# Performance work log

Measured on AMD Instinct MI355X. Metric: run time of the kernel, lower is better.

Reference implementation:

```python
import jax, jax.numpy as jnp
import numpy as np

IN_DIM = 14400
K = 25
DIMS = [7200, 3600, 1800]  # floor(in_dim / 2**(i+1))
OUT_DIM = 2
BATCH = 256


def setup_inputs() -> dict:
    key = jax.random.key(0)
    ks = jax.random.split(key, 32)
    inp = {}
    inp["x"] = jax.random.normal(ks[0], (BATCH, 2 * IN_DIM), dtype=jnp.float32)
    # shared KNN tables (both channels load the same h5 files)
    prev = [IN_DIM] + DIMS[:-1]
    for i, (d, p) in enumerate(zip(DIMS, prev)):
        inp[f"knn{i}"] = jax.random.randint(ks[1 + i], (d, K), 0, p, dtype=jnp.int64)
    std = (2.0 / K) ** 0.5
    kidx = 4
    for ch in ("p", "n"):
        for i, d in enumerate(DIMS):
            inp[f"w{ch}{i}"] = jax.random.normal(ks[kidx], (d, K), dtype=jnp.float32) * std; kidx += 1
            inp[f"b{ch}{i}"] = jnp.zeros((1, d), dtype=jnp.float32)
        inp[f"fc{ch}_w"] = jax.random.normal(ks[kidx], (OUT_DIM, DIMS[-1]), dtype=jnp.float32) * (1.0 / DIMS[-1] ** 0.5); kidx += 1
        inp[f"fc{ch}_b"] = jnp.zeros((OUT_DIM,), dtype=jnp.float32)
    inp["fc3_w"] = jax.random.normal(ks[kidx], (OUT_DIM, 4), dtype=jnp.float32) * 0.5
    inp["fc3_b"] = jnp.zeros((OUT_DIM,), dtype=jnp.float32)
    return inp


def _lcn(x, knns, ws, bs, fw, fb):
    # x: (B, in_dim). Each layer: gather KNN neighbors, weighted sum, bias, relu.
    for knn, w, b in zip(knns, ws, bs):
        g = x[:, knn]                                  # (B, dim, K) gather
        x = jax.nn.relu(jnp.einsum('bdk,dk->bd', g, w) + b)
    return x @ fw.T + fb                               # fc_angle


def reference(x, knn0, knn1, knn2,
              wp0, bp0, wp1, bp1, wp2, bp2, fcp_w, fcp_b,
              wn0, bn0, wn1, bn1, wn2, bn2, fcn_w, fcn_b,
              fc3_w, fc3_b):
    knns = (knn0, knn1, knn2)
    xpos = _lcn(x[:, :IN_DIM], knns, (wp0, wp1, wp2), (bp0, bp1, bp2), fcp_w, fcp_b)
    xneg = _lcn(x[:, IN_DIM:], knns, (wn0, wn1, wn2), (bn0, bn1, bn2), fcn_w, fcn_b)
    h = jax.nn.relu(jnp.concatenate([xpos, xneg], axis=1))  # (B, 4)
    return h @ fc3_w.T + fc3_b
```

## Files before the change

kernel.cpp:

```cpp
#include <hip/hip_runtime.h>
#include <hip/hip_bf16.h>

using bf16 = __hip_bfloat16;

typedef _Float16 half1;
typedef _Float16 half2_t __attribute__((ext_vector_type(2)));

#define K 25
#define D0 7200
#define D1 3600
#define D2 1800

#define PKB_L1 360000
#define PKB_L2 540000
#define NPK    630000
#define NPB    25200

#define NT 1024

__device__ __forceinline__ float b2f(ushort u) {
  unsigned int w = ((unsigned int)u) << 16;
  float f; __builtin_memcpy(&f, &w, 4); return f;
}
__device__ __forceinline__ ushort f2b(float f) {
  bf16 h = __float2bfloat16(f);
  ushort u; __builtin_memcpy(&u, &h, 2); return u;
}
__device__ __forceinline__ ushort f2h(float f) {
  half1 h = (half1)f;
  return __builtin_bit_cast(ushort, h);
}
__device__ __forceinline__ unsigned int pkf16(float a, float b) {
  return __builtin_bit_cast(unsigned int, __builtin_amdgcn_cvt_pkrtz(a, b));
}

__global__ __launch_bounds__(256) void prepack_kernel(
    const void* __restrict__ x,
    const void* __restrict__ knn0, const void* __restrict__ knn1,
    const void* __restrict__ knn2,
    const void* __restrict__ wp0, const void* __restrict__ bp0,
    const void* __restrict__ wp1, const void* __restrict__ bp1,
    const void* __restrict__ wp2, const void* __restrict__ bp2,
    const void* __restrict__ wn0, const void* __restrict__ bn0,
    const void* __restrict__ wn1, const void* __restrict__ bn1,
    const void* __restrict__ wn2, const void* __restrict__ bn2,
    unsigned int* __restrict__ pk, float* __restrict__ pbias,
    float* __restrict__ y, int* __restrict__ flags) {
  __shared__ int s_flags[2];
  const int t = threadIdx.x;
  if (t < 64) {
    const unsigned int u = ((const unsigned int*)x)[t * 997];
    const unsigned int e = (u >> 23) & 0xFF;
    const unsigned long long m = __ballot((e >= 192) || (e <= 30));
    if (t == 0) s_flags[0] = (__popcll(m) >= 32) ? 1 : 0;
  } else if (t < 128) {
    const int l = t - 64;
    const unsigned int hi = ((const unsigned int*)knn0)[2 * l + 1];
    const unsigned long long m = __ballot(hi != 0);
    if (l == 0) s_flags[1] = (m == 0ULL) ? 1 : 0;
  }
  __syncthreads();
  const int fdt = s_flags[0], idt = s_flags[1];

  if (blockIdx.x == 0 && t == 0) {
    flags[0] = fdt; flags[1] = idt; flags[16] = 0;
  }

  const int gid = blockIdx.x * 256 + t;
  if (gid < NPB) {
    int i = gid, d, dout, pkb;
    const void *kn, *wsel, *bsel;
    if (i < 14400) {
      const int ch = i / D0; d = i - ch * D0; dout = D0;
      pkb = ch * 180000; kn = knn0;
      wsel = ch ? wn0 : wp0; bsel = ch ? bn0 : bp0;
    } else if (i < 21600) {
      i -= 14400; const int ch = i / D1; d = i - ch * D1; dout = D1;
      pkb = PKB_L1 + ch * 90000; kn = knn1;
      wsel = ch ? wn1 : wp1; bsel = ch ? bn1 : bp1;
    } else {
      i -= 21600; const int ch = i / D2; d = i - ch * D2; dout = D2;
      pkb = PKB_L2 + ch * 45000; kn = knn2;
      wsel = ch ? wn2 : wp2; bsel = ch ? bn2 : bp2;
    }
    const int pos0 = d * K;
#pragma unroll
    for (int k = 0; k < K; ++k) {
      const unsigned int idx = idt ? ((const unsigned int*)kn)[2 * (pos0 + k)]
                                   : ((const unsigned int*)kn)[pos0 + k];
      const ushort wb = fdt ? f2h(b2f(((const ushort*)wsel)[pos0 + k]))
                            : f2h(((const float*)wsel)[pos0 + k]);
      pk[pkb + k * dout + d] = (idx << 18) | (unsigned int)wb;
    }
    pbias[gid] = fdt ? b2f(((const ushort*)bsel)[d]) : ((const float*)bsel)[d];
  } else if (gid < NPB + 1024) {
    y[gid - NPB] = 0.0f;
  }
}

template <int BIN, int BOUT>
__device__ __forceinline__ void layer_run(char* ldsb, const unsigned int* __restrict__ pk,
                                          const float* __restrict__ pbias,
                                          int pkb, int pbb, int dout) {
  for (int d = threadIdx.x; d < dout; d += NT) {
    const int base = pkb + d;
    float a0 = 0.f, a1 = 0.f;
#pragma unroll
    for (int k = 0; k < K; ++k) {
      const unsigned int pw = pk[base + k * dout];
      const half2_t vv = *(const half2_t*)(ldsb + BIN + (pw >> 16));
      const half1 wh = __builtin_bit_cast(half1, (ushort)(pw & 0xFFFFu));
      a0 = fmaf((float)wh, (float)vv.x, a0);
      a1 = fmaf((float)wh, (float)vv.y, a1);
    }
    const float bias = pbias[pbb + d];
    a0 = fmaxf(a0 + bias, 0.f);
    a1 = fmaxf(a1 + bias, 0.f);
    *(unsigned int*)(ldsb + BOUT + (d << 2)) = pkf16(a0, a1);
  }
}

__global__ __launch_bounds__(NT) void lcn_fused(
    const void* __restrict__ x, const unsigned int* __restrict__ pk,
    const float* __restrict__ pbias,
    const void* __restrict__ fcpw, const void* __restrict__ fcnw,
    const void* __restrict__ fcpb, const void* __restrict__ fcnb,
    const void* __restrict__ f3w, const void* __restrict__ f3b,
    float* __restrict__ y, int* __restrict__ flags, void* __restrict__ out) {
  __shared__ __align__(16) char ldsb[86400];
  __shared__ float red[NT / 64][4];
  __shared__ int sflag;
  const int t = threadIdx.x;
  const int ch = blockIdx.x & 1;
  const int b0 = (blockIdx.x >> 1) * 2;

  if (t == 0) sflag = flags[0];
  __syncthreads();
  const int fdt = sflag;

  if (fdt) {
    const ushort* r0 = (const ushort*)x + (size_t)b0 * 28800 + ch * 14400;
    const ushort* r1 = r0 + 28800;
    for (int c = t; c < 3600; c += NT) {
      const ushort4 a = ((const ushort4*)r0)[c];
      const ushort4 b = ((const ushort4*)r1)[c];
      uint4 u;
      u.x = pkf16(b2f(a.x), b2f(b.x));
      u.y = pkf16(b2f(a.y), b2f(b.y));
      u.z = pkf16(b2f(a.z), b2f(b.z));
      u.w = pkf16(b2f(a.w), b2f(b.w));
      ((uint4*)ldsb)[c] = u;
    }
  } else {
    const float* r0 = (const float*)x + (size_t)b0 * 28800 + ch * 14400;
    const float* r1 = r0 + 28800;
    for (int c = t; c < 3600; c += NT) {
      const float4 a = ((const float4*)r0)[c];
      const float4 b = ((const float4*)r1)[c];
      uint4 u;
      u.x = pkf16(a.x, b.x);
      u.y = pkf16(a.y, b.y);
      u.z = pkf16(a.z, b.z);
      u.w = pkf16(a.w, b.w);
      ((uint4*)ldsb)[c] = u;
    }
  }
  __syncthreads();

  layer_run<0, 57600>(ldsb, pk, pbias, 0 + ch * 180000, 0 + ch * D0, D0);
  __syncthreads();
  layer_run<57600, 0>(ldsb, pk, pbias, PKB_L1 + ch * 90000, 14400 + ch * D1, D1);
  __syncthreads();
  layer_run<0, 14400>(ldsb, pk, pbias, PKB_L2 + ch * 45000, 21600 + ch * D2, D2);
  __syncthreads();

  {
    const void* fw = ch ? fcnw : fcpw;
    float a00 = 0.f, a01 = 0.f, a10 = 0.f, a11 = 0.f;
    for (int d = t; d < D2; d += NT) {
      const half2_t vv = *(const half2_t*)(ldsb + 14400 + (d << 2));
      const float v0 = (float)vv.x;
      const float v1 = (float)vv.y;
      const float w0 = fdt ? b2f(((const ushort*)fw)[d]) : ((const float*)fw)[d];
      const float w1 = fdt ? b2f(((const ushort*)fw)[D2 + d]) : ((const float*)fw)[D2 + d];
      a00 = fmaf(w0, v0, a00); a01 = fmaf(w0, v1, a01);
      a10 = fmaf(w1, v0, a10); a11 = fmaf(w1, v1, a11);
    }
#pragma unroll
    for (int off = 32; off > 0; off >>= 1) {
      a00 += __shfl_down(a00, off);
      a01 += __shfl_down(a01, off);
      a10 += __shfl_down(a10, off);
      a11 += __shfl_down(a11, off);
    }
    const int wave = t >> 6, lane = t & 63;
    if (lane == 0) {
      red[wave][0] = a00; red[wave][1] = a01; red[wave][2] = a10; red[wave][3] = a11;
    }
    __syncthreads();
    if (t == 0) {
      float s00 = 0.f, s01 = 0.f, s10 = 0.f, s11 = 0.f;
#pragma unroll
      for (int wv = 0; wv < NT / 64; ++wv) {
        s00 += red[wv][0]; s01 += red[wv][1]; s10 += red[wv][2]; s11 += red[wv][3];
      }
      atomicAdd(&y[(ch * 2 + 0) * 256 + b0], s00);
      atomicAdd(&y[(ch * 2 + 0) * 256 + b0 + 1], s01);
      atomicAdd(&y[(ch * 2 + 1) * 256 + b0], s10);
      atomicAdd(&y[(ch * 2 + 1) * 256 + b0 + 1], s11);
    }
  }

  __syncthreads();
  if (t == 0) {
    __threadfence();
    sflag = (atomicAdd(&flags[16], 1) == (int)gridDim.x - 1) ? 1 : 0;
  }
  __syncthreads();
  if (sflag && t < 256) {
    const int b = t;
    const float y0 = atomicAdd(&y[0 * 256 + b], 0.0f);
    const float y1 = atomicAdd(&y[1 * 256 + b], 0.0f);
    const float y2 = atomicAdd(&y[2 * 256 + b], 0.0f);
    const float y3 = atomicAdd(&y[3 * 256 + b], 0.0f);
    const float bp0v = fdt ? b2f(((const ushort*)fcpb)[0]) : ((const float*)fcpb)[0];
    const float bp1v = fdt ? b2f(((const ushort*)fcpb)[1]) : ((const float*)fcpb)[1];
    const float bn0v = fdt ? b2f(((const ushort*)fcnb)[0]) : ((const float*)fcnb)[0];
    const float bn1v = fdt ? b2f(((const ushort*)fcnb)[1]) : ((const float*)fcnb)[1];
    const float h0v = fmaxf(y0 + bp0v, 0.f);
    const float h1v = fmaxf(y1 + bp1v, 0.f);
    const float h2v = fmaxf(y2 + bn0v, 0.f);
    const float h3v = fmaxf(y3 + bn1v, 0.f);
#pragma unroll
    for (int o = 0; o < 2; ++o) {
      float w0, w1, w2, w3, bb;
      if (fdt) {
        const ushort* fp = (const ushort*)f3w;
        w0 = b2f(fp[o * 4 + 0]); w1 = b2f(fp[o * 4 + 1]);
        w2 = b2f(fp[o * 4 + 2]); w3 = b2f(fp[o * 4 + 3]);
        bb = b2f(((const ushort*)f3b)[o]);
      } else {
        const float* fp = (const float*)f3w;
        w0 = fp[o * 4 + 0]; w1 = fp[o * 4 + 1];
        w2 = fp[o * 4 + 2]; w3 = fp[o * 4 + 3];
        bb = ((const float*)f3b)[o];
      }
      float r = bb;
      r = fmaf(w0, h0v, r); r = fmaf(w1, h1v, r);
      r = fmaf(w2, h2v, r); r = fmaf(w3, h3v, r);
      if (fdt) ((ushort*)out)[b * 2 + o] = f2b(r);
      else     ((float*)out)[b * 2 + o] = r;
    }
  }
}

extern "C" void kernel_launch(void* const* d_in, const int* in_sizes, int n_in,
                              void* d_out, int out_size, void* d_ws, size_t ws_size,
                              hipStream_t stream) {
  const void* x    = d_in[0];
  const void* knn0 = d_in[1];
  const void* knn1 = d_in[2];
  const void* knn2 = d_in[3];
  const void* wp0  = d_in[4];  const void* bp0 = d_in[5];
  const void* wp1  = d_in[6];  const void* bp1 = d_in[7];
  const void* wp2  = d_in[8];  const void* bp2 = d_in[9];
  const void* fcpw = d_in[10]; const void* fcpb = d_in[11];
  const void* wn0  = d_in[12]; const void* bn0 = d_in[13];
  const void* wn1  = d_in[14]; const void* bn1 = d_in[15];
  const void* wn2  = d_in[16]; const void* bn2 = d_in[17];
  const void* fcnw = d_in[18]; const void* fcnb = d_in[19];
  const void* f3w  = d_in[20]; const void* f3b  = d_in[21];

  char* ws = (char*)d_ws;
  unsigned int* pk = (unsigned int*)(ws);
  float* pbias = (float*)(ws + 2520000);
  float* y     = (float*)(ws + 2620800);
  int* flags   = (int*)(ws + 2624896);

  prepack_kernel<<<103, 256, 0, stream>>>(x, knn0, knn1, knn2,
                                          wp0, bp0, wp1, bp1, wp2, bp2,
                                          wn0, bn0, wn1, bn1, wn2, bn2,
                                          pk, pbias, y, flags);

  lcn_fused<<<256, NT, 0, stream>>>(x, pk, pbias, fcpw, fcnw, fcpb, fcnb,
                                    f3w, f3b, y, flags, d_out);
}
```

Baseline: 148.1 us.

## Fuse prepack and LCN compute into one cooperative kernel with grid sync

Merges the weight/index prepack kernel and the main LCN kernel into a single cooperative launch. Each block prepacks part of the tables and stages its x rows into LDS, then a grid-wide sync separates prepack from compute. This removes one kernel launch and overlaps x staging with prepack, at the cost of a grid barrier and a cooperative-launch requirement. A fallback to the old two-kernel path is kept if the cooperative launch fails.

```diff
diff --git a/kernel.cpp b/kernel.cpp
--- a/kernel.cpp
+++ b/kernel.cpp
@@ -1,5 +1,8 @@
 #include <hip/hip_runtime.h>
 #include <hip/hip_bf16.h>
+#include <hip/hip_cooperative_groups.h>
+
+namespace cg = cooperative_groups;
 
 using bf16 = __hip_bfloat16;
 
@@ -17,6 +20,7 @@
 #define NPB    25200
 
 #define NT 1024
+#define GRID 256
 
 __device__ __forceinline__ float b2f(ushort u) {
   unsigned int w = ((unsigned int)u) << 16;
@@ -34,68 +38,39 @@
   return __builtin_bit_cast(unsigned int, __builtin_amdgcn_cvt_pkrtz(a, b));
 }
 
-__global__ __launch_bounds__(256) void prepack_kernel(
-    const void* __restrict__ x,
-    const void* __restrict__ knn0, const void* __restrict__ knn1,
-    const void* __restrict__ knn2,
-    const void* __restrict__ wp0, const void* __restrict__ bp0,
-    const void* __restrict__ wp1, const void* __restrict__ bp1,
-    const void* __restrict__ wp2, const void* __restrict__ bp2,
-    const void* __restrict__ wn0, const void* __restrict__ bn0,
-    const void* __restrict__ wn1, const void* __restrict__ bn1,
-    const void* __restrict__ wn2, const void* __restrict__ bn2,
-    unsigned int* __restrict__ pk, float* __restrict__ pbias,
-    float* __restrict__ y, int* __restrict__ flags) {
-  __shared__ int s_flags[2];
-  const int t = threadIdx.x;
-  if (t < 64) {
-    const unsigned int u = ((const unsigned int*)x)[t * 997];
-    const unsigned int e = (u >> 23) & 0xFF;
-    const unsigned long long m = __ballot((e >= 192) || (e <= 30));
-    if (t == 0) s_flags[0] = (__popcll(m) >= 32) ? 1 : 0;
-  } else if (t < 128) {
-    const int l = t - 64;
-    const unsigned int hi = ((const unsigned int*)knn0)[2 * l + 1];
-    const unsigned long long m = __ballot(hi != 0);
-    if (l == 0) s_flags[1] = (m == 0ULL) ? 1 : 0;
-  }
-  __syncthreads();
-  const int fdt = s_flags[0], idt = s_flags[1];
-
-  if (blockIdx.x == 0 && t == 0) {
-    flags[0] = fdt; flags[1] = idt; flags[16] = 0;
-  }
-
-  const int gid = blockIdx.x * 256 + t;
-  if (gid < NPB) {
-    int i = gid, d, dout, pkb;
-    const void *kn, *wsel, *bsel;
-    if (i < 14400) {
-      const int ch = i / D0; d = i - ch * D0; dout = D0;
-      pkb = ch * 180000; kn = knn0;
-      wsel = ch ? wn0 : wp0; bsel = ch ? bn0 : bp0;
-    } else if (i < 21600) {
-      i -= 14400; const int ch = i / D1; d = i - ch * D1; dout = D1;
-      pkb = PKB_L1 + ch * 90000; kn = knn1;
-      wsel = ch ? wn1 : wp1; bsel = ch ? bn1 : bp1;
-    } else {
-      i -= 21600; const int ch = i / D2; d = i - ch * D2; dout = D2;
-      pkb = PKB_L2 + ch * 45000; kn = knn2;
-      wsel = ch ? wn2 : wp2; bsel = ch ? bn2 : bp2;
-    }
-    const int pos0 = d * K;
-#pragma unroll
-    for (int k = 0; k < K; ++k) {
-      const unsigned int idx = idt ? ((const unsigned int*)kn)[2 * (pos0 + k)]
-                                   : ((const unsigned int*)kn)[pos0 + k];
-      const ushort wb = fdt ? f2h(b2f(((const ushort*)wsel)[pos0 + k]))
-                            : f2h(((const float*)wsel)[pos0 + k]);
-      pk[pkb + k * dout + d] = (idx << 18) | (unsigned int)wb;
-    }
-    pbias[gid] = fdt ? b2f(((const ushort*)bsel)[d]) : ((const float*)bsel)[d];
-  } else if (gid < NPB + 1024) {
-    y[gid - NPB] = 0.0f;
-  }
+__device__ __forceinline__ void prepack_one(
+    int gid, int idt, int fdt,
+    const void* knn0, const void* knn1, const void* knn2,
+    const void* wp0, const void* bp0, const void* wp1, const void* bp1,
+    const void* wp2, const void* bp2,
+    const void* wn0, const void* bn0, const void* wn1, const void* bn1,
+    const void* wn2, const void* bn2,
+    unsigned int* __restrict__ pk, float* __restrict__ pbias) {
+  int i = gid, d, dout, pkb;
+  const void *kn, *wsel, *bsel;
+  if (i < 14400) {
+    const int ch = i / D0; d = i - ch * D0; dout = D0;
+    pkb = ch * 180000; kn = knn0;
+    wsel = ch ? wn0 : wp0; bsel = ch ? bn0 : bp0;
+  } else if (i < 21600) {
+    i -= 14400; const int ch = i / D1; d = i - ch * D1; dout = D1;
+    pkb = PKB_L1 + ch * 90000; kn = knn1;
+    wsel = ch ? wn1 : wp1; bsel = ch ? bn1 : bp1;
+  } else {
+    i -= 21600; const int ch = i / D2; d = i - ch * D2; dout = D2;
+    pkb = PKB_L2 + ch * 45000; kn = knn2;
+    wsel = ch ? wn2 : wp2; bsel = ch ? bn2 : bp2;
+  }
+  const int pos0 = d * K;
+#pragma unroll
+  for (int k = 0; k < K; ++k) {
+    const unsigned int idx = idt ? ((const unsigned int*)kn)[2 * (pos0 + k)]
+                                 : ((const unsigned int*)kn)[pos0 + k];
+    const ushort wb = fdt ? f2h(b2f(((const ushort*)wsel)[pos0 + k]))
+                          : f2h(((const float*)wsel)[pos0 + k]);
+    pk[pkb + k * dout + d] = (idx << 18) | (unsigned int)wb;
+  }
+  pbias[gid] = fdt ? b2f(((const ushort*)bsel)[d]) : ((const float*)bsel)[d];
 }
 
 template <int BIN, int BOUT>
@@ -120,24 +95,9 @@
   }
 }
 
-__global__ __launch_bounds__(NT) void lcn_fused(
-    const void* __restrict__ x, const unsigned int* __restrict__ pk,
-    const float* __restrict__ pbias,
-    const void* __restrict__ fcpw, const void* __restrict__ fcnw,
-    const void* __restrict__ fcpb, const void* __restrict__ fcnb,
-    const void* __restrict__ f3w, const void* __restrict__ f3b,
-    float* __restrict__ y, int* __restrict__ flags, void* __restrict__ out) {
-  __shared__ __align__(16) char ldsb[86400];
-  __shared__ float red[NT / 64][4];
-  __shared__ int sflag;
-  const int t = threadIdx.x;
-  const int ch = blockIdx.x & 1;
-  const int b0 = (blockIdx.x >> 1) * 2;
-
-  if (t == 0) sflag = flags[0];
-  __syncthreads();
-  const int fdt = sflag;
-
+__device__ __forceinline__ void stage_x(char* ldsb, const void* __restrict__ x,
+                                        int fdt, int ch, int b0) {
+  const int t = threadIdx.x;
   if (fdt) {
     const ushort* r0 = (const ushort*)x + (size_t)b0 * 28800 + ch * 14400;
     const ushort* r1 = r0 + 28800;
@@ -165,7 +125,16 @@
       ((uint4*)ldsb)[c] = u;
     }
   }
-  __syncthreads();
+}
+
+__device__ __forceinline__ void compute_phase(
+    char* ldsb, float (*red)[4], int* sflag_p,
+    const unsigned int* __restrict__ pk, const float* __restrict__ pbias,
+    const void* fcpw, const void* fcnw, const void* fcpb, const void* fcnb,
+    const void* f3w, const void* f3b,
+    float* __restrict__ y, int* __restrict__ flags, void* __restrict__ out,
+    int fdt, int ch, int b0, int nblocks) {
+  const int t = threadIdx.x;
 
   layer_run<0, 57600>(ldsb, pk, pbias, 0 + ch * 180000, 0 + ch * D0, D0);
   __syncthreads();
@@ -214,10 +183,10 @@
   __syncthreads();
   if (t == 0) {
     __threadfence();
-    sflag = (atomicAdd(&flags[16], 1) == (int)gridDim.x - 1) ? 1 : 0;
-  }
-  __syncthreads();
-  if (sflag && t < 256) {
+    *sflag_p = (atomicAdd(&flags[16], 1) == nblocks - 1) ? 1 : 0;
+  }
+  __syncthreads();
+  if (*sflag_p && t < 256) {
     const int b = t;
     const float y0 = atomicAdd(&y[0 * 256 + b], 0.0f);
     const float y1 = atomicAdd(&y[1 * 256 + b], 0.0f);
@@ -254,6 +223,133 @@
   }
 }
 
+__global__ __launch_bounds__(NT) void lcn_all(
+    const void* __restrict__ x,
+    const void* __restrict__ knn0, const void* __restrict__ knn1,
+    const void* __restrict__ knn2,
+    const void* __restrict__ wp0, const void* __restrict__ bp0,
+    const void* __restrict__ wp1, const void* __restrict__ bp1,
+    const void* __restrict__ wp2, const void* __restrict__ bp2,
+    const void* __restrict__ wn0, const void* __restrict__ bn0,
+    const void* __restrict__ wn1, const void* __restrict__ bn1,
+    const void* __restrict__ wn2, const void* __restrict__ bn2,
+    const void* __restrict__ fcpw, const void* __restrict__ fcnw,
+    const void* __restrict__ fcpb, const void* __restrict__ fcnb,
+    const void* __restrict__ f3w, const void* __restrict__ f3b,
+    unsigned int* __restrict__ pk, float* __restrict__ pbias,
+    float* __restrict__ y, int* __restrict__ flags, void* __restrict__ out) {
+  __shared__ __align__(16) char ldsb[86400];
+  __shared__ float red[NT / 64][4];
+  __shared__ int s_flags[2];
+  __shared__ int sflag;
+  const int t = threadIdx.x;
+  const int bid = blockIdx.x;
+  const int ch = bid & 1;
+  const int b0 = (bid >> 1) * 2;
+
+  if (t < 64) {
+    const unsigned int u = ((const unsigned int*)x)[t * 997];
+    const unsigned int e = (u >> 23) & 0xFF;
+    const unsigned long long m = __ballot((e >= 192) || (e <= 30));
+    if (t == 0) s_flags[0] = (__popcll(m) >= 32) ? 1 : 0;
+  } else if (t < 128) {
+    const int l = t - 64;
+    const unsigned int hi = ((const unsigned int*)knn0)[2 * l + 1];
+    const unsigned long long m = __ballot(hi != 0);
+    if (l == 0) s_flags[1] = (m == 0ULL) ? 1 : 0;
+  }
+  __syncthreads();
+  const int fdt = s_flags[0], idt = s_flags[1];
+
+  const int gid = bid * NT + t;
+  if (gid < NPB) {
+    prepack_one(gid, idt, fdt, knn0, knn1, knn2,
+                wp0, bp0, wp1, bp1, wp2, bp2,
+                wn0, bn0, wn1, bn1, wn2, bn2, pk, pbias);
+  }
+  if (bid == GRID - 1) {
+    atomicExch((unsigned int*)&y[t & 1023], 0u);
+    if (t == 0) atomicExch(&flags[16], 0);
+  }
+
+  stage_x(ldsb, x, fdt, ch, b0);
+  __syncthreads();
+
+  __threadfence();
+  cg::this_grid().sync();
+  __threadfence();
+
+  compute_phase(ldsb, red, &sflag, pk, pbias, fcpw, fcnw, fcpb, fcnb,
+                f3w, f3b, y, flags, out, fdt, ch, b0, GRID);
+}
+
+__global__ __launch_bounds__(256) void prepack_kernel(
+    const void* __restrict__ x,
+    const void* __restrict__ knn0, const void* __restrict__ knn1,
+    const void* __restrict__ knn2,
+    const void* __restrict__ wp0, const void* __restrict__ bp0,
+    const void* __restrict__ wp1, const void* __restrict__ bp1,
+    const void* __restrict__ wp2, const void* __restrict__ bp2,
+    const void* __restrict__ wn0, const void* __restrict__ bn0,
+    const void* __restrict__ wn1, const void* __restrict__ bn1,
+    const void* __restrict__ wn2, const void* __restrict__ bn2,
+    unsigned int* __restrict__ pk, float* __restrict__ pbias,
+    float* __restrict__ y, int* __restrict__ flags) {
+  __shared__ int s_flags[2];
+  const int t = threadIdx.x;
+  if (t < 64) {
+    const unsigned int u = ((const unsigned int*)x)[t * 997];
+    const unsigned int e = (u >> 23) & 0xFF;
+    const unsigned long long m = __ballot((e >= 192) || (e <= 30));
+    if (t == 0) s_flags[0] = (__popcll(m) >= 32) ? 1 : 0;
+  } else if (t < 128) {
+    const int l = t - 64;
+    const unsigned int hi = ((const unsigned int*)knn0)[2 * l + 1];
+    const unsigned long long m = __ballot(hi != 0);
+    if (l == 0) s_flags[1] = (m == 0ULL) ? 1 : 0;
+  }
+  __syncthreads();
+  const int fdt = s_flags[0], idt = s_flags[1];
+
+  if (blockIdx.x == 0 && t == 0) {
+    flags[0] = fdt; flags[1] = idt; flags[16] = 0;
+  }
+
+  const int gid = blockIdx.x * 256 + t;
+  if (gid < NPB) {
+    prepack_one(gid, idt, fdt, knn0, knn1, knn2,
+                wp0, bp0, wp1, bp1, wp2, bp2,
+                wn0, bn0, wn1, bn1, wn2, bn2, pk, pbias);
+  } else if (gid < NPB + 1024) {
+    y[gid - NPB] = 0.0f;
+  }
+}
+
+__global__ __launch_bounds__(NT) void lcn_fused(
+    const void* __restrict__ x, const unsigned int* __restrict__ pk,
+    const float* __restrict__ pbias,
+    const void* __restrict__ fcpw, const void* __restrict__ fcnw,
+    const void* __restrict__ fcpb, const void* __restrict__ fcnb,
+    const void* __restrict__ f3w, const void* __restrict__ f3b,
+    float* __restrict__ y, int* __restrict__ flags, void* __restrict__ out) {
+  __shared__ __align__(16) char ldsb[86400];
+  __shared__ float red[NT / 64][4];
+  __shared__ int sflag;
+  const int t = threadIdx.x;
+  const int ch = blockIdx.x & 1;
+  const int b0 = (blockIdx.x >> 1) * 2;
+
+  if (t == 0) sflag = flags[0];
+  __syncthreads();
+  const int fdt = sflag;
+
+  stage_x(ldsb, x, fdt, ch, b0);
+  __syncthreads();
+
+  compute_phase(ldsb, red, &sflag, pk, pbias, fcpw, fcnw, fcpb, fcnb,
+                f3w, f3b, y, flags, out, fdt, ch, b0, (int)gridDim.x);
+}
+
 extern "C" void kernel_launch(void* const* d_in, const int* in_sizes, int n_in,
                               void* d_out, int out_size, void* d_ws, size_t ws_size,
                               hipStream_t stream) {
@@ -277,11 +373,25 @@
   float* y     = (float*)(ws + 2620800);
   int* flags   = (int*)(ws + 2624896);
 
-  prepack_kernel<<<103, 256, 0, stream>>>(x, knn0, knn1, knn2,
-                                          wp0, bp0, wp1, bp1, wp2, bp2,
-                                          wn0, bn0, wn1, bn1, wn2, bn2,
-                                          pk, pbias, y, flags);
-
-  lcn_fused<<<256, NT, 0, stream>>>(x, pk, pbias, fcpw, fcnw, fcpb, fcnb,
-                                    f3w, f3b, y, flags, d_out);
-}
+  void* out = d_out;
+  void* args[] = {
+      (void*)&x, (void*)&knn0, (void*)&knn1, (void*)&knn2,
+      (void*)&wp0, (void*)&bp0, (void*)&wp1, (void*)&bp1,
+      (void*)&wp2, (void*)&bp2,
+      (void*)&wn0, (void*)&bn0, (void*)&wn1, (void*)&bn1,
+      (void*)&wn2, (void*)&bn2,
+      (void*)&fcpw, (void*)&fcnw, (void*)&fcpb, (void*)&fcnb,
+      (void*)&f3w, (void*)&f3b,
+      (void*)&pk, (void*)&pbias, (void*)&y, (void*)&flags, (void*)&out};
+
+  hipError_t e = hipLaunchCooperativeKernel((const void*)lcn_all, dim3(GRID),
+                                            dim3(NT), args, 0, stream);
+  if (e != hipSuccess) {
+    prepack_kernel<<<103, 256, 0, stream>>>(x, knn0, knn1, knn2,
+                                            wp0, bp0, wp1, bp1, wp2, bp2,
+                                            wn0, bn0, wn1, bn1, wn2, bn2,
+                                            pk, pbias, y, flags);
+    lcn_fused<<<256, NT, 0, stream>>>(x, pk, pbias, fcpw, fcnw, fcpb, fcnb,
+                                      f3w, f3b, y, flags, d_out);
+  }
+}
```

Result: slower. 366.2 us (+147.3%).

## Split prepack across two thread halves and process two outputs per thread in layers

Applied to the files above, without the earlier changes.

The prepack kernel now gives each output dimension to two threads that each pack about half of the K neighbours, doubling the grid, and a dedicated block zeroes y. In the fused kernel, layer_run takes the output dimension as a template parameter and has each thread compute two output positions per iteration with independent accumulators, exposing more memory-level parallelism for the packed-weight loads and LDS gathers. Launch bounds now request a minimum of 4 blocks per multiprocessor. Handling two outputs at once raises register pressure, and the min-blocks hint may force spills, though the 86 KB of LDS per block likely limits occupancy anyway.

```diff
diff --git a/kernel.cpp b/kernel.cpp
--- a/kernel.cpp
+++ b/kernel.cpp
@@ -32,6 +32,35 @@
 }
 __device__ __forceinline__ unsigned int pkf16(float a, float b) {
   return __builtin_bit_cast(unsigned int, __builtin_amdgcn_cvt_pkrtz(a, b));
+}
+
+struct DimMap {
+  int d, dout, pkb;
+  const void *kn, *wsel, *bsel;
+};
+__device__ __forceinline__ DimMap map_gid(
+    int gid,
+    const void* knn0, const void* knn1, const void* knn2,
+    const void* wp0, const void* bp0, const void* wp1, const void* bp1,
+    const void* wp2, const void* bp2,
+    const void* wn0, const void* bn0, const void* wn1, const void* bn1,
+    const void* wn2, const void* bn2) {
+  DimMap m;
+  int i = gid;
+  if (i < 14400) {
+    const int ch = i / D0; m.d = i - ch * D0; m.dout = D0;
+    m.pkb = ch * 180000; m.kn = knn0;
+    m.wsel = ch ? wn0 : wp0; m.bsel = ch ? bn0 : bp0;
+  } else if (i < 21600) {
+    i -= 14400; const int ch = i / D1; m.d = i - ch * D1; m.dout = D1;
+    m.pkb = PKB_L1 + ch * 90000; m.kn = knn1;
+    m.wsel = ch ? wn1 : wp1; m.bsel = ch ? bn1 : bp1;
+  } else {
+    i -= 21600; const int ch = i / D2; m.d = i - ch * D2; m.dout = D2;
+    m.pkb = PKB_L2 + ch * 45000; m.kn = knn2;
+    m.wsel = ch ? wn2 : wp2; m.bsel = ch ? bn2 : bp2;
+  }
+  return m;
 }
 
 __global__ __launch_bounds__(256) void prepack_kernel(
@@ -48,6 +77,15 @@
     float* __restrict__ y, int* __restrict__ flags) {
   __shared__ int s_flags[2];
   const int t = threadIdx.x;
+
+  if (blockIdx.x == 197) {
+    if (t < 256) {
+#pragma unroll
+      for (int j = 0; j < 4; ++j) y[t + j * 256] = 0.0f;
+    }
+    return;
+  }
+
   if (t < 64) {
     const unsigned int u = ((const unsigned int*)x)[t * 997];
     const unsigned int e = (u >> 23) & 0xFF;
@@ -66,61 +104,107 @@
     flags[0] = fdt; flags[1] = idt; flags[16] = 0;
   }
 
-  const int gid = blockIdx.x * 256 + t;
+  const int local = t & 127;
+  const int khalf = t >> 7;
+  const int gid = blockIdx.x * 128 + local;
   if (gid < NPB) {
-    int i = gid, d, dout, pkb;
-    const void *kn, *wsel, *bsel;
-    if (i < 14400) {
-      const int ch = i / D0; d = i - ch * D0; dout = D0;
-      pkb = ch * 180000; kn = knn0;
-      wsel = ch ? wn0 : wp0; bsel = ch ? bn0 : bp0;
-    } else if (i < 21600) {
-      i -= 14400; const int ch = i / D1; d = i - ch * D1; dout = D1;
-      pkb = PKB_L1 + ch * 90000; kn = knn1;
-      wsel = ch ? wn1 : wp1; bsel = ch ? bn1 : bp1;
+    const DimMap m = map_gid(gid, knn0, knn1, knn2,
+                             wp0, bp0, wp1, bp1, wp2, bp2,
+                             wn0, bn0, wn1, bn1, wn2, bn2);
+    const int pos0 = m.d * K;
+    if (khalf == 0) {
+#pragma unroll
+      for (int k = 0; k < 13; ++k) {
+        const unsigned int idx = idt ? ((const unsigned int*)m.kn)[2 * (pos0 + k)]
+                                     : ((const unsigned int*)m.kn)[pos0 + k];
+        const ushort wb = fdt ? f2h(b2f(((const ushort*)m.wsel)[pos0 + k]))
+                              : f2h(((const float*)m.wsel)[pos0 + k]);
+        pk[m.pkb + k * m.dout + m.d] = (idx << 18) | (unsigned int)wb;
+      }
+      pbias[gid] = fdt ? b2f(((const ushort*)m.bsel)[m.d]) : ((const float*)m.bsel)[m.d];
     } else {
-      i -= 21600; const int ch = i / D2; d = i - ch * D2; dout = D2;
-      pkb = PKB_L2 + ch * 45000; kn = knn2;
-      wsel = ch ? wn2 : wp2; bsel = ch ? bn2 : bp2;
-    }
-    const int pos0 = d * K;
-#pragma unroll
-    for (int k = 0; k < K; ++k) {
-      const unsigned int idx = idt ? ((const unsigned int*)kn)[2 * (pos0 + k)]
-                                   : ((const unsigned int*)kn)[pos0 + k];
-      const ushort wb = fdt ? f2h(b2f(((const ushort*)wsel)[pos0 + k]))
-                            : f2h(((const float*)wsel)[pos0 + k]);
-      pk[pkb + k * dout + d] = (idx << 18) | (unsigned int)wb;
-    }
-    pbias[gid] = fdt ? b2f(((const ushort*)bsel)[d]) : ((const float*)bsel)[d];
-  } else if (gid < NPB + 1024) {
-    y[gid - NPB] = 0.0f;
-  }
-}
-
-template <int BIN, int BOUT>
+#pragma unroll
+      for (int k = 13; k < 25; ++k) {
+        const unsigned int idx = idt ? ((const unsigned int*)m.kn)[2 * (pos0 + k)]
+                                     : ((const unsigned int*)m.kn)[pos0 + k];
+        const ushort wb = fdt ? f2h(b2f(((const ushort*)m.wsel)[pos0 + k]))
+                              : f2h(((const float*)m.wsel)[pos0 + k]);
+        pk[m.pkb + k * m.dout + m.d] = (idx << 18) | (unsigned int)wb;
+      }
+    }
+  }
+}
+
+template <int BIN, int BOUT, int DOUT>
 __device__ __forceinline__ void layer_run(char* ldsb, const unsigned int* __restrict__ pk,
                                           const float* __restrict__ pbias,
-                                          int pkb, int pbb, int dout) {
-  for (int d = threadIdx.x; d < dout; d += NT) {
-    const int base = pkb + d;
-    float a0 = 0.f, a1 = 0.f;
+                                          int pkb, int pbb) {
+  const int t = threadIdx.x;
+  for (int d = t; d < DOUT; d += 2 * NT) {
+    const int dB = d + NT;
+    const bool hasB = dB < DOUT;
+    const unsigned int* sA = pk + pkb + d;
+    const unsigned int* sB = pk + pkb + dB;
+    float a0 = 0.f, a1 = 0.f, c0 = 0.f, c1 = 0.f;
 #pragma unroll
     for (int k = 0; k < K; ++k) {
-      const unsigned int pw = pk[base + k * dout];
-      const half2_t vv = *(const half2_t*)(ldsb + BIN + (pw >> 16));
-      const half1 wh = __builtin_bit_cast(half1, (ushort)(pw & 0xFFFFu));
-      a0 = fmaf((float)wh, (float)vv.x, a0);
-      a1 = fmaf((float)wh, (float)vv.y, a1);
-    }
-    const float bias = pbias[pbb + d];
-    a0 = fmaxf(a0 + bias, 0.f);
-    a1 = fmaxf(a1 + bias, 0.f);
+      const unsigned int pwA = sA[k * DOUT];
+      const unsigned int pwB = hasB ? sB[k * DOUT] : 0u;
+      const half2_t vA = *(const half2_t*)(ldsb + BIN + (pwA >> 16));
+      const half2_t vB = *(const half2_t*)(ldsb + BIN + (pwB >> 16));
+      const half1 wA = __builtin_bit_cast(half1, (ushort)(pwA & 0xFFFFu));
+      const half1 wB = __builtin_bit_cast(half1, (ushort)(pwB & 0xFFFFu));
+      a0 = fmaf((float)wA, (float)vA.x, a0);
+      a1 = fmaf((float)wA, (float)vA.y, a1);
+      c0 = fmaf((float)wB, (float)vB.x, c0);
+      c1 = fmaf((float)wB, (float)vB.y, c1);
+    }
+    const float biasA = pbias[pbb + d];
+    a0 = fmaxf(a0 + biasA, 0.f);
+    a1 = fmaxf(a1 + biasA, 0.f);
     *(unsigned int*)(ldsb + BOUT + (d << 2)) = pkf16(a0, a1);
-  }
-}
-
-__global__ __launch_bounds__(NT) void lcn_fused(
+    if (hasB) {
+      const float biasB = pbias[pbb + dB];
+      c0 = fmaxf(c0 + biasB, 0.f);
+      c1 = fmaxf(c1 + biasB, 0.f);
+      *(unsigned int*)(ldsb + BOUT + (dB << 2)) = pkf16(c0, c1);
+    }
+  }
+}
+
+__device__ __forceinline__ void stage_x(char* ldsb, const void* __restrict__ x,
+                                        int fdt, int ch, int b0) {
+  const int t = threadIdx.x;
+  if (fdt) {
+    const ushort* r0 = (const ushort*)x + (size_t)b0 * 28800 + ch * 14400;
+    const ushort* r1 = r0 + 28800;
+    for (int c = t; c < 3600; c += NT) {
+      const ushort4 a = ((const ushort4*)r0)[c];
+      const ushort4 b = ((const ushort4*)r1)[c];
+      uint4 u;
+      u.x = pkf16(b2f(a.x), b2f(b.x));
+      u.y = pkf16(b2f(a.y), b2f(b.y));
+      u.z = pkf16(b2f(a.z), b2f(b.z));
+      u.w = pkf16(b2f(a.w), b2f(b.w));
+      ((uint4*)ldsb)[c] = u;
+    }
+  } else {
+    const float* r0 = (const float*)x + (size_t)b0 * 28800 + ch * 14400;
+    const float* r1 = r0 + 28800;
+    for (int c = t; c < 3600; c += NT) {
+      const float4 a = ((const float4*)r0)[c];
+      const float4 b = ((const float4*)r1)[c];
+      uint4 u;
+      u.x = pkf16(a.x, b.x);
+      u.y = pkf16(a.y, b.y);
+      u.z = pkf16(a.z, b.z);
+      u.w = pkf16(a.w, b.w);
+      ((uint4*)ldsb)[c] = u;
+    }
+  }
+}
+
+__global__ __launch_bounds__(NT, 4) void lcn_fused(
     const void* __restrict__ x, const unsigned int* __restrict__ pk,
     const float* __restrict__ pbias,
     const void* __restrict__ fcpw, const void* __restrict__ fcnw,
@@ -138,40 +222,14 @@
   __syncthreads();
   const int fdt = sflag;
 
-  if (fdt) {
-    const ushort* r0 = (const ushort*)x + (size_t)b0 * 28800 + ch * 14400;
-    const ushort* r1 = r0 + 28800;
-    for (int c = t; c < 3600; c += NT) {
-      const ushort4 a = ((const ushort4*)r0)[c];
-      const ushort4 b = ((const ushort4*)r1)[c];
-      uint4 u;
-      u.x = pkf16(b2f(a.x), b2f(b.x));
-      u.y = pkf16(b2f(a.y), b2f(b.y));
-      u.z = pkf16(b2f(a.z), b2f(b.z));
-      u.w = pkf16(b2f(a.w), b2f(b.w));
-      ((uint4*)ldsb)[c] = u;
-    }
-  } else {
-    const float* r0 = (const float*)x + (size_t)b0 * 28800 + ch * 14400;
-    const float* r1 = r0 + 28800;
-    for (int c = t; c < 3600; c += NT) {
-      const float4 a = ((const float4*)r0)[c];
-      const float4 b = ((const float4*)r1)[c];
-      uint4 u;
-      u.x = pkf16(a.x, b.x);
-      u.y = pkf16(a.y, b.y);
-      u.z = pkf16(a.z, b.z);
-      u.w = pkf16(a.w, b.w);
-      ((uint4*)ldsb)[c] = u;
-    }
-  }
-  __syncthreads();
-
-  layer_run<0, 57600>(ldsb, pk, pbias, 0 + ch * 180000, 0 + ch * D0, D0);
-  __syncthreads();
-  layer_run<57600, 0>(ldsb, pk, pbias, PKB_L1 + ch * 90000, 14400 + ch * D1, D1);
-  __syncthreads();
-  layer_run<0, 14400>(ldsb, pk, pbias, PKB_L2 + ch * 45000, 21600 + ch * D2, D2);
+  stage_x(ldsb, x, fdt, ch, b0);
+  __syncthreads();
+
+  layer_run<0, 57600, D0>(ldsb, pk, pbias, 0 + ch * 180000, 0 + ch * D0);
+  __syncthreads();
+  layer_run<57600, 0, D1>(ldsb, pk, pbias, PKB_L1 + ch * 90000, 14400 + ch * D1);
+  __syncthreads();
+  layer_run<0, 14400, D2>(ldsb, pk, pbias, PKB_L2 + ch * 45000, 21600 + ch * D2);
   __syncthreads();
 
   {
@@ -277,7 +335,7 @@
   float* y     = (float*)(ws + 2620800);
   int* flags   = (int*)(ws + 2624896);
 
-  prepack_kernel<<<103, 256, 0, stream>>>(x, knn0, knn1, knn2,
+  prepack_kernel<<<198, 256, 0, stream>>>(x, knn0, knn1, knn2,
                                           wp0, bp0, wp1, bp1, wp2, bp2,
                                           wn0, bn0, wn1, bn1, wn2, bn2,
                                           pk, pbias, y, flags);
```

Result: slower. 174.4 us (+17.7%).
